# Performance work log

Hardware: AMD Instinct MI355X
Metric: run time of the kernel (lower is better)

## Reference

```python
import jax, jax.numpy as jnp
import numpy as np

B, N, F, H, M, EF, OUT = 256, 32, 40, 100, 100, 4, 128
MESSAGE_PASSES = 3


def setup_inputs() -> dict:
    key = jax.random.key(0)
    ks = jax.random.split(key, 8)
    # Deterministic ring graphs: node i <-> node (i+1)%N, one-hot bond type.
    # Every node has degree 2 -> static nonzero counts.
    rng = np.random.default_rng(0)
    edges = np.zeros((B, N, N, EF), np.float32)
    b = np.arange(B)[:, None]
    i = np.arange(N)[None, :]
    j = (i + 1) % N
    t = rng.integers(0, EF, size=(B, N))
    edges[b, i, j, t] = 1.0
    edges[b, j, i, t] = 1.0

    nodes = jax.random.normal(ks[0], (B, N, F), jnp.float32)

    def init(k, shape, fan):
        return jax.random.normal(k, shape, jnp.float32) / np.sqrt(fan).astype(np.float32)

    W_msg = init(ks[1], (M, H, EF), H)          # MNN edge-conditioned weights
    W_ih = init(ks[2], (3 * H, M), M)            # GRUCell input weights
    W_hh = init(ks[3], (3 * H, H), H)            # GRUCell hidden weights
    b_ih = jnp.zeros((3 * H,), jnp.float32)
    b_hh = jnp.zeros((3 * H,), jnp.float32)
    Wg = init(ks[4], (H + F, H), H + F)          # gather gate
    bg = jnp.zeros((H,), jnp.float32)
    We = init(ks[5], (H, H), H)                  # gather embed
    be = jnp.zeros((H,), jnp.float32)
    Wo = init(ks[6], (H, OUT), H)                # output head
    bo = jnp.zeros((OUT,), jnp.float32)

    return {
        "nodes": nodes, "edges": jnp.asarray(edges),
        "W_msg": W_msg, "W_ih": W_ih, "W_hh": W_hh, "b_ih": b_ih, "b_hh": b_hh,
        "Wg": Wg, "bg": bg, "We": We, "be": be, "Wo": Wo, "bo": bo,
        "n_edges": B * N * 2, "n_node_entries": B * N,
    }


def gru_cell(x, h, W_ih, W_hh, b_ih, b_hh):
    gi = x @ W_ih.T + b_ih
    gh = h @ W_hh.T + b_hh
    ir, iz, inn = jnp.split(gi, 3, axis=-1)
    hr, hz, hn = jnp.split(gh, 3, axis=-1)
    r = jax.nn.sigmoid(ir + hr)
    z = jax.nn.sigmoid(iz + hz)
    n = jnp.tanh(inn + r * hn)
    return (1.0 - z) * n + z * h


def reference(nodes, edges, W_msg, W_ih, W_hh, b_ih, b_hh, Wg, bg, We, be, Wo, bo,
              n_edges, n_node_entries):
    adjacency = jnp.sum(edges, axis=3)                      # (B, N, N)
    eb, en, eg = jnp.nonzero(adjacency, size=n_edges)       # edge-level indices
    nb, nn_ = jnp.nonzero(adjacency.sum(-1), size=n_node_entries)

    # Dense one-hot segment-sum matrix: (n_node_entries, n_edges)
    same = (nb[:, None] == eb) & (nn_[:, None] == en)
    msg_sum_mat = same.astype(jnp.float32)

    edge_batch_edges = edges[eb, en, eg, :]                 # (E, EF)

    hidden = jnp.zeros((B, N, H), jnp.float32).at[:, :, :F].set(nodes)
    node_h = hidden[nb, nn_, :]                             # (V, H)

    for _ in range(MESSAGE_PASSES):
        nghb_h = hidden[eb, eg, :]                          # (E, H)
        # MNN message: sum_f edges[e,f] * W_msg[m,h,f] * nghb[e,h]
        message_terms = jnp.einsum('ef,mhf,eh->em', edge_batch_edges, W_msg, nghb_h)
        messages = msg_sum_mat @ message_terms              # (V, M) dense one-hot matmul
        node_h = gru_cell(messages, node_h, W_ih, W_hh, b_ih, b_hh)
        hidden = hidden.at[nb, nn_, :].set(node_h)

    node_mask = (adjacency.sum(-1) != 0).astype(jnp.float32)  # (B, N)
    cat = jnp.concatenate([hidden, nodes], axis=-1)           # (B, N, H+F)
    gate = jax.nn.sigmoid(cat @ Wg + bg)
    emb = gate * (hidden @ We + be)
    graph_emb = jnp.sum(emb * node_mask[..., None], axis=1)   # (B, H)
    return graph_emb @ Wo + bo                                # (B, OUT)
```

## Files before the change

### kernel.cpp

```cpp
#include <hip/hip_runtime.h>
#include <cstddef>
#include <cstdint>

#define B_   256
#define N_   32
#define F_   40
#define H_   100
#define OUT_ 128
#define TB   1024
#define XCS  168
#define XMS  136
#define ST2  40
#define NBLK 343
#define NLO  63

using bf16x8 = __attribute__((ext_vector_type(8))) short;
using f32x4  = __attribute__((ext_vector_type(4))) float;

#define MFMA(a,b,c) __builtin_amdgcn_mfma_f32_16x16x32_bf16((a),(b),(c),0,0,0)

__device__ __forceinline__ float sigmoidf_(float x){ return 1.0f/(1.0f+__expf(-x)); }
__device__ __forceinline__ float tanhf_(float x){
  float e = __expf(2.0f*x);
  return 1.0f - 2.0f/(e+1.0f);
}
__device__ __forceinline__ float bf2f(short s){ return __uint_as_float(((uint32_t)(uint16_t)s)<<16); }
__device__ __forceinline__ short f2bf(float x){
  uint32_t u = __float_as_uint(x);
  return (short)((u + 0x7FFFu + ((u>>16)&1u))>>16);
}
__device__ __forceinline__ void bsplit(float x, short& hi, short& lo){
  hi = f2bf(x);
  lo = f2bf(x - bf2f(hi));
}

__global__ void prep_frags4(const float* __restrict__ Wmsg,
                            const float* __restrict__ Wih,
                            const float* __restrict__ Whh,
                            const float* __restrict__ Wg,
                            const float* __restrict__ We,
                            short* __restrict__ AFhi,
                            short* __restrict__ AFlo){
  int slot = blockIdx.x*blockDim.x + threadIdx.x;
  if (slot >= NBLK*512) return;
  int blk = slot>>9, r = slot&511, lane = r>>3, jj = r&7;
  int m = lane&15, q = lane>>4, kl = q*8+jj;
  float v = 0.0f;
  if (blk < 112){
    int t = blk/28, rem = blk%28, jmt = rem>>2, ks = rem&3;
    int mg = jmt*16+m, h = ks*32+kl;
    if (mg<100 && h<100) v = Wmsg[(mg*100+h)*4 + t];
    AFhi[slot] = f2bf(v);
  } else if (blk < 280){
    int bb = blk-112, mat = bb/28, rem = bb%28, jmt = rem>>2, ks = rem&3;
    int mg = jmt*16+m, k = ks*32+kl;
    if (mg<100 && k<100)
      v = (mat<3) ? Wih[(mat*100+mg)*100+k] : Whh[((mat-3)*100+mg)*100+k];
    AFhi[slot] = f2bf(v);
  } else if (blk < 315){
    int bb = blk-280, jmt = bb/5, ks = bb%5;
    int mg = jmt*16+m, k = ks*32+kl;
    if (mg<100 && k<140) v = Wg[k*100+mg];
    short hi,lo; bsplit(v,hi,lo);
    AFhi[slot] = hi;
    AFlo[(size_t)(blk-280)*512 + r] = lo;
  } else {
    int bb = blk-315, jmt = bb>>2, ks = bb&3;
    int mg = jmt*16+m, k = ks*32+kl;
    if (mg<100 && k<100) v = We[k*100+mg];
    short hi,lo; bsplit(v,hi,lo);
    AFhi[slot] = hi;
    AFlo[(size_t)(blk-280)*512 + r] = lo;
  }
}

__global__ __launch_bounds__(TB, 4) void mpnn_mfma(
    const float* __restrict__ nodes, const float* __restrict__ edges,
    const short* __restrict__ AFhi, const short* __restrict__ AFlo,
    const float* __restrict__ b_ih, const float* __restrict__ b_hh,
    const float* __restrict__ bg, const float* __restrict__ be,
    const float* __restrict__ Wo, const float* __restrict__ bo,
    float* __restrict__ out){
  const int b = blockIdx.x;
  const int tid = threadIdx.x;
  const int lane = tid & 63;
  const int w = tid >> 6;

  __shared__ short XcH[32*XCS], XcL[32*XCS];
  __shared__ short XcT[112*ST2];
  __shared__ short XmH[32*XMS];
  __shared__ short XyH[4][32*XMS];
  __shared__ short Aw[4][32*32];
  __shared__ float sh_ge[H_];
  __shared__ float sh_part[4][OUT_];
  __shared__ float sh_rowsum[N_];

  for (int i=tid;i<(32*XCS)/2;i+=TB){ ((int*)XcH)[i]=0; ((int*)XcL)[i]=0; }
  for (int i=tid;i<(32*XMS)/2;i+=TB){ ((int*)XmH)[i]=0; }
  for (int i=tid;i<(112*ST2)/2;i+=TB){ ((int*)XcT)[i]=0; }
  for (int i=tid;i<(4*32*XMS)/2;i+=TB){ ((int*)XyH)[i]=0; }
  if (tid < H_) sh_ge[tid]=0.0f;
  if (tid < N_) sh_rowsum[tid]=0.0f;
  __syncthreads();

  {
    int n = tid>>5, g = tid&31;
    const float4 ev = *(const float4*)(edges + (((size_t)b*N_+n)*N_+g)*4);
    float adj = ev.x+ev.y+ev.z+ev.w;
    if (adj != 0.0f) atomicAdd(&sh_rowsum[n], adj);
    Aw[0][n*32+g] = f2bf(ev.x);
    Aw[1][n*32+g] = f2bf(ev.y);
    Aw[2][n*32+g] = f2bf(ev.z);
    Aw[3][n*32+g] = f2bf(ev.w);
  }
  for (int p=tid; p<N_*F_; p+=TB){
    int n = p/F_, f = p%F_;
    float x = nodes[((size_t)b*N_+n)*F_ + f];
    short hi,lo; bsplit(x,hi,lo);
    XcH[n*XCS+f]=hi;      XcL[n*XCS+f]=lo;
    XcH[n*XCS+100+f]=hi;
    XcT[f*ST2+n]=hi;
  }
  __syncthreads();

  const int jmt = w>>1, nt = w&1;
  const bool task = (w < 14);
  const int nrow = nt*16 + (lane&15);
  const int boff = (lane>>4)*8;

  for (int pass=0; pass<3; ++pass){
    if (task){
      bf16x8 at = *(const bf16x8*)&XcT[(jmt*16+(lane&15))*ST2 + boff];
      int kbase = jmt*16 + boff/2;
#pragma unroll
      for (int t=0;t<4;++t){
        bf16x8 bt = *(const bf16x8*)&Aw[t][nrow*32 + boff];
        f32x4 D = (f32x4)0.0f;
        D = MFMA(at, bt, D);
        short4 pk;
        pk.x = f2bf(D[0]); pk.y = f2bf(D[1]);
        pk.z = f2bf(D[2]); pk.w = f2bf(D[3]);
        *(short4*)&XyH[t][nrow*XMS + kbase] = pk;
      }
    }
    __syncthreads();
    f32x4 Ch0=(f32x4)0.0f, Ch1=(f32x4)0.0f, Ch2=(f32x4)0.0f;
    if (task){
      f32x4 Cm=(f32x4)0.0f;
#pragma unroll 1
      for (int t=0;t<4;++t){
        const short* pa = AFhi + ((size_t)(t*28 + jmt*4))*512 + lane*8;
        const short* pb = XyH[t] + nrow*XMS + boff;
        bf16x8 a0 = *(const bf16x8*)(pa);
        bf16x8 a1 = *(const bf16x8*)(pa+512);
        bf16x8 a2 = *(const bf16x8*)(pa+1024);
        bf16x8 a3 = *(const bf16x8*)(pa+1536);
        bf16x8 b0 = *(const bf16x8*)(pb);
        bf16x8 b1 = *(const bf16x8*)(pb+32);
        bf16x8 b2 = *(const bf16x8*)(pb+64);
        bf16x8 b3 = *(const bf16x8*)(pb+96);
        Cm = MFMA(a0,b0,Cm); Cm = MFMA(a1,b1,Cm);
        Cm = MFMA(a2,b2,Cm); Cm = MFMA(a3,b3,Cm);
      }
      {
        const short* pb = XcH + nrow*XCS + boff;
        bf16x8 b0 = *(const bf16x8*)(pb);
        bf16x8 b1 = *(const bf16x8*)(pb+32);
        bf16x8 b2 = *(const bf16x8*)(pb+64);
        bf16x8 b3 = *(const bf16x8*)(pb+96);
        const short* pa = AFhi + ((size_t)(112 + 3*28 + jmt*4))*512 + lane*8;
        {
          bf16x8 a0=*(const bf16x8*)(pa),      a1=*(const bf16x8*)(pa+512);
          bf16x8 a2=*(const bf16x8*)(pa+1024), a3=*(const bf16x8*)(pa+1536);
          Ch0 = MFMA(a0,b0,Ch0); Ch0 = MFMA(a1,b1,Ch0);
          Ch0 = MFMA(a2,b2,Ch0); Ch0 = MFMA(a3,b3,Ch0);
        }
        pa += 28*512;
        {
          bf16x8 a0=*(const bf16x8*)(pa),      a1=*(const bf16x8*)(pa+512);
          bf16x8 a2=*(const bf16x8*)(pa+1024), a3=*(const bf16x8*)(pa+1536);
          Ch1 = MFMA(a0,b0,Ch1); Ch1 = MFMA(a1,b1,Ch1);
          Ch1 = MFMA(a2,b2,Ch1); Ch1 = MFMA(a3,b3,Ch1);
        }
        pa += 28*512;
        {
          bf16x8 a0=*(const bf16x8*)(pa),      a1=*(const bf16x8*)(pa+512);
          bf16x8 a2=*(const bf16x8*)(pa+1024), a3=*(const bf16x8*)(pa+1536);
          Ch2 = MFMA(a0,b0,Ch2); Ch2 = MFMA(a1,b1,Ch2);
          Ch2 = MFMA(a2,b2,Ch2); Ch2 = MFMA(a3,b3,Ch2);
        }
      }
      for (int r=0;r<4;++r){
        int row = jmt*16 + (lane>>4)*4 + r;
        if (row<100) XmH[nrow*XMS+row] = f2bf(Cm[r]);
      }
    }
    __syncthreads();
    if (task){
      f32x4 Ci0=(f32x4)0.0f, Ci1=(f32x4)0.0f, Ci2=(f32x4)0.0f;
      {
        const short* pb = XmH + nrow*XMS + boff;
        bf16x8 b0 = *(const bf16x8*)(pb);
        bf16x8 b1 = *(const bf16x8*)(pb+32);
        bf16x8 b2 = *(const bf16x8*)(pb+64);
        bf16x8 b3 = *(const bf16x8*)(pb+96);
        const short* pa = AFhi + ((size_t)(112 + jmt*4))*512 + lane*8;
        {
          bf16x8 a0=*(const bf16x8*)(pa),      a1=*(const bf16x8*)(pa+512);
          bf16x8 a2=*(const bf16x8*)(pa+1024), a3=*(const bf16x8*)(pa+1536);
          Ci0 = MFMA(a0,b0,Ci0); Ci0 = MFMA(a1,b1,Ci0);
          Ci0 = MFMA(a2,b2,Ci0); Ci0 = MFMA(a3,b3,Ci0);
        }
        pa += 28*512;
        {
          bf16x8 a0=*(const bf16x8*)(pa),      a1=*(const bf16x8*)(pa+512);
          bf16x8 a2=*(const bf16x8*)(pa+1024), a3=*(const bf16x8*)(pa+1536);
          Ci1 = MFMA(a0,b0,Ci1); Ci1 = MFMA(a1,b1,Ci1);
          Ci1 = MFMA(a2,b2,Ci1); Ci1 = MFMA(a3,b3,Ci1);
        }
        pa += 28*512;
        {
          bf16x8 a0=*(const bf16x8*)(pa),      a1=*(const bf16x8*)(pa+512);
          bf16x8 a2=*(const bf16x8*)(pa+1024), a3=*(const bf16x8*)(pa+1536);
          Ci2 = MFMA(a0,b0,Ci2); Ci2 = MFMA(a1,b1,Ci2);
          Ci2 = MFMA(a2,b2,Ci2); Ci2 = MFMA(a3,b3,Ci2);
        }
      }
      bool msk = (sh_rowsum[nrow] != 0.0f);
#pragma unroll
      for (int r=0;r<4;++r){
        int row = jmt*16 + (lane>>4)*4 + r;
        if (row<100){
          float ho = bf2f(XcH[nrow*XCS+row]) + bf2f(XcL[nrow*XCS+row]);
          float rr = sigmoidf_(Ci0[r]+Ch0[r] + b_ih[row]     + b_hh[row]);
          float zz = sigmoidf_(Ci1[r]+Ch1[r] + b_ih[100+row] + b_hh[100+row]);
          float nn = tanhf_(Ci2[r] + b_ih[200+row] + rr*(Ch2[r] + b_hh[200+row]));
          float hnew = (1.0f-zz)*nn + zz*ho;
          if (!msk) hnew = ho;
          short hi,lo; bsplit(hnew,hi,lo);
          XcH[nrow*XCS+row]=hi; XcL[nrow*XCS+row]=lo;
          XcT[row*ST2+nrow]=hi;
        }
      }
    }
    __syncthreads();
  }

  f32x4 Cg=(f32x4)0.0f, Ce=(f32x4)0.0f;
  if (task){
    const short* pb = XcH + nrow*XCS + boff;
    bf16x8 b0 = *(const bf16x8*)(pb);
    bf16x8 b1 = *(const bf16x8*)(pb+32);
    bf16x8 b2 = *(const bf16x8*)(pb+64);
    bf16x8 b3 = *(const bf16x8*)(pb+96);
    bf16x8 b4 = *(const bf16x8*)(pb+128);
    {
      const short* ph = AFhi + ((size_t)(280 + jmt*5))*512 + lane*8;
      const short* pl = AFlo + ((size_t)(jmt*5))*512 + lane*8;
      Cg = MFMA(*(const bf16x8*)(ph),      b0, Cg);
      Cg = MFMA(*(const bf16x8*)(pl),      b0, Cg);
      Cg = MFMA(*(const bf16x8*)(ph+512),  b1, Cg);
      Cg = MFMA(*(const bf16x8*)(pl+512),  b1, Cg);
      Cg = MFMA(*(const bf16x8*)(ph+1024), b2, Cg);
      Cg = MFMA(*(const bf16x8*)(pl+1024), b2, Cg);
      Cg = MFMA(*(const bf16x8*)(ph+1536), b3, Cg);
      Cg = MFMA(*(const bf16x8*)(pl+1536), b3, Cg);
      Cg = MFMA(*(const bf16x8*)(ph+2048), b4, Cg);
      Cg = MFMA(*(const bf16x8*)(pl+2048), b4, Cg);
    }
    {
      const short* ph = AFhi + ((size_t)(315 + jmt*4))*512 + lane*8;
      const short* pl = AFlo + ((size_t)(35 + jmt*4))*512 + lane*8;
      Ce = MFMA(*(const bf16x8*)(ph),      b0, Ce);
      Ce = MFMA(*(const bf16x8*)(pl),      b0, Ce);
      Ce = MFMA(*(const bf16x8*)(ph+512),  b1, Ce);
      Ce = MFMA(*(const bf16x8*)(pl+512),  b1, Ce);
      Ce = MFMA(*(const bf16x8*)(ph+1024), b2, Ce);
      Ce = MFMA(*(const bf16x8*)(pl+1024), b2, Ce);
      Ce = MFMA(*(const bf16x8*)(ph+1536), b3, Ce);
      Ce = MFMA(*(const bf16x8*)(pl+1536), b3, Ce);
    }
    bool msk = (sh_rowsum[nrow] != 0.0f);
#pragma unroll
    for (int r=0;r<4;++r){
      int row = jmt*16 + (lane>>4)*4 + r;
      float v = 0.0f;
      if (row<100){
        float gate = sigmoidf_(Cg[r] + bg[row]);
        float emb  = gate*(Ce[r] + be[row]);
        v = msk ? emb : 0.0f;
      }
      v += __shfl_xor(v, 1);
      v += __shfl_xor(v, 2);
      v += __shfl_xor(v, 4);
      v += __shfl_xor(v, 8);
      if (row<100 && (lane&15)==0) atomicAdd(&sh_ge[row], v);
    }
  }
  __syncthreads();
  if (tid < 512){
    int o = tid & 127, q = tid >> 7;
    float s = 0.0f;
    int k0 = 25*q;
#pragma unroll 5
    for (int k=k0; k<k0+25; ++k) s += sh_ge[k]*Wo[k*OUT_+o];
    sh_part[q][o] = s;
  }
  __syncthreads();
  if (tid < OUT_){
    out[(size_t)b*OUT_ + tid] = bo[tid] + sh_part[0][tid] + sh_part[1][tid]
                              + sh_part[2][tid] + sh_part[3][tid];
  }
}

extern "C" void kernel_launch(void* const* d_in, const int* in_sizes, int n_in,
                              void* d_out, int out_size, void* d_ws, size_t ws_size,
                              hipStream_t stream){
  const float* nodes = (const float*)d_in[0];
  const float* edges = (const float*)d_in[1];
  const float* W_msg = (const float*)d_in[2];
  const float* W_ih  = (const float*)d_in[3];
  const float* W_hh  = (const float*)d_in[4];
  const float* b_ih  = (const float*)d_in[5];
  const float* b_hh  = (const float*)d_in[6];
  const float* Wg    = (const float*)d_in[7];
  const float* bg    = (const float*)d_in[8];
  const float* We    = (const float*)d_in[9];
  const float* be    = (const float*)d_in[10];
  const float* Wo    = (const float*)d_in[11];
  const float* bo    = (const float*)d_in[12];

  short* AFhi = (short*)d_ws;
  short* AFlo = AFhi + (size_t)NBLK*512;

  prep_frags4<<<(NBLK*512 + 255)/256, 256, 0, stream>>>(W_msg, W_ih, W_hh, Wg, We,
                                                        AFhi, AFlo);
  mpnn_mfma<<<B_, TB, 0, stream>>>(nodes, edges, AFhi, AFlo, b_ih, b_hh, bg, be,
                                   Wo, bo, (float*)d_out);
}
```

Baseline: 114.5 us.

## Keep fp32 hidden state in registers and move Wh matmul before first barrier

Drops the low-half bf16 shared buffer for the hidden state and keeps the exact fp32 hidden value per lane in registers across passes. The hidden-gate MFMAs (W_hh·h) now run in the first phase alongside the adjacency product, which spreads MFMA work across the barriers. Writes to XmH and XcH become packed short4 stores. This cuts LDS traffic and footprint, at the cost of more live registers across the pass loop.

```diff
diff --git a/kernel.cpp b/kernel.cpp
--- a/kernel.cpp
+++ b/kernel.cpp
@@ -86,7 +86,7 @@
   const int lane = tid & 63;
   const int w = tid >> 6;
 
-  __shared__ short XcH[32*XCS], XcL[32*XCS];
+  __shared__ short XcH[32*XCS];
   __shared__ short XcT[112*ST2];
   __shared__ short XmH[32*XMS];
   __shared__ short XyH[4][32*XMS];
@@ -95,7 +95,7 @@
   __shared__ float sh_part[4][OUT_];
   __shared__ float sh_rowsum[N_];
 
-  for (int i=tid;i<(32*XCS)/2;i+=TB){ ((int*)XcH)[i]=0; ((int*)XcL)[i]=0; }
+  for (int i=tid;i<(32*XCS)/2;i+=TB){ ((int*)XcH)[i]=0; }
   for (int i=tid;i<(32*XMS)/2;i+=TB){ ((int*)XmH)[i]=0; }
   for (int i=tid;i<(112*ST2)/2;i+=TB){ ((int*)XcT)[i]=0; }
   for (int i=tid;i<(4*32*XMS)/2;i+=TB){ ((int*)XyH)[i]=0; }
@@ -116,35 +116,75 @@
   for (int p=tid; p<N_*F_; p+=TB){
     int n = p/F_, f = p%F_;
     float x = nodes[((size_t)b*N_+n)*F_ + f];
-    short hi,lo; bsplit(x,hi,lo);
-    XcH[n*XCS+f]=hi;      XcL[n*XCS+f]=lo;
+    short hi = f2bf(x);
+    XcH[n*XCS+f]=hi;
     XcH[n*XCS+100+f]=hi;
     XcT[f*ST2+n]=hi;
   }
-  __syncthreads();
 
   const int jmt = w>>1, nt = w&1;
   const bool task = (w < 14);
   const int nrow = nt*16 + (lane&15);
   const int boff = (lane>>4)*8;
+  const int rowbase = jmt*16 + (lane>>4)*4;
+
+  float hst[4] = {0.f,0.f,0.f,0.f};
+  if (task){
+#pragma unroll
+    for (int r=0;r<4;++r){
+      int row = rowbase + r;
+      if (row < F_) hst[r] = nodes[((size_t)b*N_+nrow)*F_ + row];
+    }
+  }
+  __syncthreads();
 
   for (int pass=0; pass<3; ++pass){
+    f32x4 Ch0=(f32x4)0.0f, Ch1=(f32x4)0.0f, Ch2=(f32x4)0.0f;
     if (task){
-      bf16x8 at = *(const bf16x8*)&XcT[(jmt*16+(lane&15))*ST2 + boff];
-      int kbase = jmt*16 + boff/2;
+      {
+        bf16x8 at = *(const bf16x8*)&XcT[(jmt*16+(lane&15))*ST2 + boff];
+        int kbase = jmt*16 + (boff>>1);
 #pragma unroll
-      for (int t=0;t<4;++t){
-        bf16x8 bt = *(const bf16x8*)&Aw[t][nrow*32 + boff];
-        f32x4 D = (f32x4)0.0f;
-        D = MFMA(at, bt, D);
-        short4 pk;
-        pk.x = f2bf(D[0]); pk.y = f2bf(D[1]);
-        pk.z = f2bf(D[2]); pk.w = f2bf(D[3]);
-        *(short4*)&XyH[t][nrow*XMS + kbase] = pk;
+        for (int t=0;t<4;++t){
+          bf16x8 bt = *(const bf16x8*)&Aw[t][nrow*32 + boff];
+          f32x4 D = (f32x4)0.0f;
+          D = MFMA(at, bt, D);
+          short4 pk;
+          pk.x = f2bf(D[0]); pk.y = f2bf(D[1]);
+          pk.z = f2bf(D[2]); pk.w = f2bf(D[3]);
+          *(short4*)&XyH[t][nrow*XMS + kbase] = pk;
+        }
+      }
+      {
+        const short* pb = XcH + nrow*XCS + boff;
+        bf16x8 b0 = *(const bf16x8*)(pb);
+        bf16x8 b1 = *(const bf16x8*)(pb+32);
+        bf16x8 b2 = *(const bf16x8*)(pb+64);
+        bf16x8 b3 = *(const bf16x8*)(pb+96);
+        const short* pa = AFhi + ((size_t)(112 + 3*28 + jmt*4))*512 + lane*8;
+        {
+          bf16x8 a0=*(const bf16x8*)(pa),      a1=*(const bf16x8*)(pa+512);
+          bf16x8 a2=*(const bf16x8*)(pa+1024), a3=*(const bf16x8*)(pa+1536);
+          Ch0 = MFMA(a0,b0,Ch0); Ch0 = MFMA(a1,b1,Ch0);
+          Ch0 = MFMA(a2,b2,Ch0); Ch0 = MFMA(a3,b3,Ch0);
+        }
+        pa += 28*512;
+        {
+          bf16x8 a0=*(const bf16x8*)(pa),      a1=*(const bf16x8*)(pa+512);
+          bf16x8 a2=*(const bf16x8*)(pa+1024), a3=*(const bf16x8*)(pa+1536);
+          Ch1 = MFMA(a0,b0,Ch1); Ch1 = MFMA(a1,b1,Ch1);
+          Ch1 = MFMA(a2,b2,Ch1); Ch1 = MFMA(a3,b3,Ch1);
+        }
+        pa += 28*512;
+        {
+          bf16x8 a0=*(const bf16x8*)(pa),      a1=*(const bf16x8*)(pa+512);
+          bf16x8 a2=*(const bf16x8*)(pa+1024), a3=*(const bf16x8*)(pa+1536);
+          Ch2 = MFMA(a0,b0,Ch2); Ch2 = MFMA(a1,b1,Ch2);
+          Ch2 = MFMA(a2,b2,Ch2); Ch2 = MFMA(a3,b3,Ch2);
+        }
       }
     }
     __syncthreads();
-    f32x4 Ch0=(f32x4)0.0f, Ch1=(f32x4)0.0f, Ch2=(f32x4)0.0f;
     if (task){
       f32x4 Cm=(f32x4)0.0f;
 #pragma unroll 1
@@ -162,37 +202,11 @@
         Cm = MFMA(a0,b0,Cm); Cm = MFMA(a1,b1,Cm);
         Cm = MFMA(a2,b2,Cm); Cm = MFMA(a3,b3,Cm);
       }
-      {
-        const short* pb = XcH + nrow*XCS + boff;
-        bf16x8 b0 = *(const bf16x8*)(pb);
-        bf16x8 b1 = *(const bf16x8*)(pb+32);
-        bf16x8 b2 = *(const bf16x8*)(pb+64);
-        bf16x8 b3 = *(const bf16x8*)(pb+96);
-        const short* pa = AFhi + ((size_t)(112 + 3*28 + jmt*4))*512 + lane*8;
-        {
-          bf16x8 a0=*(const bf16x8*)(pa),      a1=*(const bf16x8*)(pa+512);
-          bf16x8 a2=*(const bf16x8*)(pa+1024), a3=*(const bf16x8*)(pa+1536);
-          Ch0 = MFMA(a0,b0,Ch0); Ch0 = MFMA(a1,b1,Ch0);
-          Ch0 = MFMA(a2,b2,Ch0); Ch0 = MFMA(a3,b3,Ch0);
-        }
-        pa += 28*512;
-        {
-          bf16x8 a0=*(const bf16x8*)(pa),      a1=*(const bf16x8*)(pa+512);
-          bf16x8 a2=*(const bf16x8*)(pa+1024), a3=*(const bf16x8*)(pa+1536);
-          Ch1 = MFMA(a0,b0,Ch1); Ch1 = MFMA(a1,b1,Ch1);
-          Ch1 = MFMA(a2,b2,Ch1); Ch1 = MFMA(a3,b3,Ch1);
-        }
-        pa += 28*512;
-        {
-          bf16x8 a0=*(const bf16x8*)(pa),      a1=*(const bf16x8*)(pa+512);
-          bf16x8 a2=*(const bf16x8*)(pa+1024), a3=*(const bf16x8*)(pa+1536);
-          Ch2 = MFMA(a0,b0,Ch2); Ch2 = MFMA(a1,b1,Ch2);
-          Ch2 = MFMA(a2,b2,Ch2); Ch2 = MFMA(a3,b3,Ch2);
-        }
-      }
-      for (int r=0;r<4;++r){
-        int row = jmt*16 + (lane>>4)*4 + r;
-        if (row<100) XmH[nrow*XMS+row] = f2bf(Cm[r]);
+      if (rowbase < 100){
+        short4 pk;
+        pk.x = f2bf(Cm[0]); pk.y = f2bf(Cm[1]);
+        pk.z = f2bf(Cm[2]); pk.w = f2bf(Cm[3]);
+        *(short4*)&XmH[nrow*XMS + rowbase] = pk;
       }
     }
     __syncthreads();
@@ -226,21 +240,24 @@
           Ci2 = MFMA(a2,b2,Ci2); Ci2 = MFMA(a3,b3,Ci2);
         }
       }
-      bool msk = (sh_rowsum[nrow] != 0.0f);
+      if (rowbase < 100){
+        bool msk = (sh_rowsum[nrow] != 0.0f);
+        short4 pk;
 #pragma unroll
-      for (int r=0;r<4;++r){
-        int row = jmt*16 + (lane>>4)*4 + r;
-        if (row<100){
-          float ho = bf2f(XcH[nrow*XCS+row]) + bf2f(XcL[nrow*XCS+row]);
+        for (int r=0;r<4;++r){
+          int row = rowbase + r;
+          float ho = hst[r];
           float rr = sigmoidf_(Ci0[r]+Ch0[r] + b_ih[row]     + b_hh[row]);
           float zz = sigmoidf_(Ci1[r]+Ch1[r] + b_ih[100+row] + b_hh[100+row]);
           float nn = tanhf_(Ci2[r] + b_ih[200+row] + rr*(Ch2[r] + b_hh[200+row]));
           float hnew = (1.0f-zz)*nn + zz*ho;
           if (!msk) hnew = ho;
-          short hi,lo; bsplit(hnew,hi,lo);
-          XcH[nrow*XCS+row]=hi; XcL[nrow*XCS+row]=lo;
-          XcT[row*ST2+nrow]=hi;
-        }
+          hst[r] = hnew;
+          short hb = f2bf(hnew);
+          ((short*)&pk)[r] = hb;
+          XcT[row*ST2+nrow] = hb;
+        }
+        *(short4*)&XcH[nrow*XCS + rowbase] = pk;
       }
     }
     __syncthreads();
@@ -283,7 +300,7 @@
     bool msk = (sh_rowsum[nrow] != 0.0f);
 #pragma unroll
     for (int r=0;r<4;++r){
-      int row = jmt*16 + (lane>>4)*4 + r;
+      int row = rowbase + r;
       float v = 0.0f;
       if (row<100){
         float gate = sigmoidf_(Cg[r] + bg[row]);
```

Result: no change. 113.0 us (-1.3%).
